# Optimization experiments

Measured on AMD Instinct MI355X. Metric: run time of the kernel, lower is better.

Reference implementation:

```python
import jax, jax.numpy as jnp
import numpy as np

NUM_HEADS = 4
D_K = 64
D_MODEL = NUM_HEADS * D_K  # 256
SEN_LEN = 8192
N_GROUPS = 4096
BASE_LEN = 64
N_EDGES = N_GROUPS * BASE_LEN  # 262144
PATH_LEN = 64


def setup_inputs() -> dict:
    rng = np.random.default_rng(0)
    key = jax.random.key(0)
    ks = jax.random.split(key, 16)

    # ragged group lengths, each >= 2, summing exactly to N_EDGES
    half = N_GROUPS // 2
    r = rng.integers(-(BASE_LEN - 2), BASE_LEN - 1, size=half)
    edge_len = np.concatenate([BASE_LEN + r, BASE_LEN - r]).astype(np.int64)
    assert edge_len.sum() == N_EDGES and edge_len.min() >= 2

    # distinct token ids; include src=0 and tar=1 so path_agg branches fire
    perm = rng.permutation(np.arange(2, SEN_LEN))[: N_GROUPS - 2]
    token_ids = np.concatenate([np.array([0, 1]), perm]).astype(np.int64)

    def w(k, shape):
        return jax.random.normal(k, shape, jnp.float32) / np.sqrt(shape[-1]).astype(np.float32)

    return {
        "path": jax.random.normal(ks[0], (PATH_LEN, D_MODEL), jnp.float32),
        "path_len": PATH_LEN,
        "q": jax.random.normal(ks[1], (SEN_LEN, D_MODEL), jnp.float32),
        "k": jax.random.normal(ks[2], (N_EDGES, D_MODEL), jnp.float32),
        "v": jax.random.normal(ks[3], (N_EDGES, D_MODEL), jnp.float32),
        "graphs": 0,
        "edge_len": jnp.asarray(edge_len),
        "token_ids": jnp.asarray(token_ids),
        "pair": jnp.array([0, 1], jnp.int32),
        "rev": 0,
        "W_qpair": w(ks[4], (D_MODEL, 2 * D_MODEL)),
        "W_pk": w(ks[5], (D_MODEL, D_MODEL)),
        "W_pv": w(ks[6], (D_MODEL, D_MODEL)),
        "W_q": w(ks[7], (D_MODEL, D_MODEL)),
        "W_k": w(ks[8], (D_MODEL, D_MODEL)),
        "W_v": w(ks[9], (D_MODEL, D_MODEL)),
        "W_out": w(ks[10], (D_MODEL, D_MODEL)),
        "b_out": jnp.zeros((D_MODEL,), jnp.float32),
        "W_agg": w(ks[11], (D_MODEL, 2 * D_MODEL)),
    }


def _forward(path, q, k, v, edge_len, token_ids, pair, rev,
             W_qpair, W_pk, W_pv, W_q, W_k, W_v, W_out, b_out, W_agg):
    H, dk = NUM_HEADS, D_K
    G = edge_len.shape[0]
    E = k.shape[0]
    scale = 1.0 / jnp.sqrt(jnp.float32(dk))

    src = pair[0] if rev == 0 else pair[1]
    tar = pair[1] if rev == 0 else pair[0]

    # pair query: cat(q[src], q[tar]) -> linear -> [H, 1, dk]
    pair_q = (jnp.concatenate([q[src], q[tar]]) @ W_qpair.T).reshape(1, H, dk).transpose(1, 0, 2)

    qh = (q @ W_q.T).reshape(-1, H, dk).transpose(1, 0, 2)      # [H, S, dk]
    pk = (path @ W_pk.T).reshape(-1, H, dk).transpose(1, 0, 2)  # [H, P, dk]
    pv = (path @ W_pv.T).reshape(-1, H, dk).transpose(1, 0, 2)  # [H, P, dk]
    kh = (k @ W_k.T).reshape(-1, H, dk).transpose(1, 0, 2)      # [H, E, dk]
    vh = (v @ W_v.T).reshape(-1, H, dk).transpose(1, 0, 2)      # [H, E, dk]

    # ---- pair/path attention ----
    att = jax.nn.softmax(jnp.einsum('hqd,hpd->hqp', pair_q, pk) * scale, axis=-1)  # [H,1,P]
    path_vals = jnp.einsum('hqp,hpd->hqd', att, pv).sum(axis=1)  # [H, dk]
    path_result = path_vals.reshape(-1) @ W_out.T + b_out        # [d_model]

    # ---- segmented per-group attention (vectorized ragged loop) ----
    seg = jnp.repeat(jnp.arange(G), edge_len, total_repeat_length=E)  # [E]
    q_sel = qh[:, token_ids, :]          # [H, G, dk] query per group
    qe = q_sel[:, seg, :]                # [H, E, dk] query per edge
    # torch.matmul(q_[H,dk], k_[H,i,dk].T) broadcasts to cross-head logits [a,b,i]
    logits = jnp.einsum('aed,bed->eab', qe, kh) * scale  # [E, H, H]
    lmax = jax.lax.stop_gradient(jax.ops.segment_max(logits, seg, num_segments=G))
    ex = jnp.exp(logits - lmax[seg])
    denom = jax.ops.segment_sum(ex, seg, num_segments=G)
    p = ex / denom[seg]                                   # segmented softmax [E, H, H]
    # sum over key-head b per edge, then segment-reduce over edges of each group
    out_e = jnp.einsum('eab,bed->ead', p, vh)             # [E, H, dk]
    hid = jax.ops.segment_sum(out_e, seg, num_segments=G) # [G, H, dk]
    new_hid = hid.reshape(G, H * dk) @ W_out.T + b_out    # [G, d_model] (dropout=identity)

    # ---- assemble output rows ----
    pr = jnp.broadcast_to(path_result, (G, D_MODEL))
    feat_path = jnp.concatenate([new_hid, pr], axis=1) @ W_agg.T  # token == src
    path_feat = jnp.concatenate([pr, new_hid], axis=1) @ W_agg.T  # token == tar
    is_src = (token_ids == src)[:, None]
    is_tar = (token_ids == tar)[:, None]
    vals = jnp.where(is_src, feat_path, jnp.where(is_tar, path_feat, new_hid))
    returned = q.at[token_ids].set(vals)
    return returned, att


def reference(path, path_len, q, k, v, graphs, edge_len, token_ids, pair, rev,
              W_qpair, W_pk, W_pv, W_q, W_k, W_v, W_out, b_out, W_agg):
    return _forward(path, q, k, v, edge_len, token_ids, pair, rev,
                    W_qpair, W_pk, W_pv, W_q, W_k, W_v, W_out, b_out, W_agg)
```

## Files before the change

### kernel.cpp

```cpp
#include <hip/hip_runtime.h>
#include <hip/hip_bf16.h>

#define H 4
#define DK 64
#define DM 256
#define SEN 8192
#define NG 4096
#define ETOT 262144
#define PLEN 64
#define MAXE 128

typedef unsigned short ushortT;
typedef __attribute__((ext_vector_type(8))) __bf16 bf16x8;
typedef __attribute__((ext_vector_type(8))) unsigned short us8;
typedef __attribute__((ext_vector_type(4))) unsigned short us4;
typedef __attribute__((ext_vector_type(4))) float f32x4;

#define TMS 264
#define KVS 260

__device__ __forceinline__ ushortT f2bf(float f) {
    unsigned u = __float_as_uint(f);
    u += 0x7FFF + ((u >> 16) & 1);
    return (ushortT)(u >> 16);
}
__device__ __forceinline__ bf16x8 ldb8(const ushortT* p) {
    us8 v = *(const us8*)p;
    return __builtin_bit_cast(bf16x8, v);
}
__device__ __forceinline__ bf16x8 pack8(const float* f) {
    us8 v;
#pragma unroll
    for (int j = 0; j < 8; j++) v[j] = f2bf(f[j]);
    return __builtin_bit_cast(bf16x8, v);
}
__device__ __forceinline__ ushortT sbf(float f) {
    return __builtin_bit_cast(ushortT, (__bf16)f);
}
__device__ __forceinline__ __bf16 u2b(ushortT u) {
    return __builtin_bit_cast(__bf16, u);
}
__device__ __forceinline__ bf16x8 pack8f(float4 a, float4 b) {
    bf16x8 r;
    r[0] = (__bf16)a.x; r[1] = (__bf16)a.y; r[2] = (__bf16)a.z; r[3] = (__bf16)a.w;
    r[4] = (__bf16)b.x; r[5] = (__bf16)b.y; r[6] = (__bf16)b.z; r[7] = (__bf16)b.w;
    return r;
}

__global__ __launch_bounds__(256) void scan_kernel(const int* __restrict__ edge_len,
                                                   int* __restrict__ starts) {
    __shared__ int part[256];
    const int tid = threadIdx.x;
    const int base = tid * 16;
    int loc[16];
    int s = 0;
#pragma unroll
    for (int i = 0; i < 16; i++) { loc[i] = s; s += edge_len[base + i]; }
    part[tid] = s;
    __syncthreads();
    if (tid == 0) {
        int acc = 0;
        for (int i = 0; i < 256; i++) { int t = part[i]; part[i] = acc; acc += t; }
    }
    __syncthreads();
    const int off = part[tid];
#pragma unroll
    for (int i = 0; i < 16; i++) starts[base + i] = off + loc[i];
}

__global__ void copy_kernel(const float* __restrict__ q, float* __restrict__ out) {
    const size_t i = (size_t)blockIdx.x * blockDim.x + threadIdx.x;
    ((float4*)out)[i] = ((const float4*)q)[i];
}

__global__ __launch_bounds__(256) void wprep_kernel(
    const float* __restrict__ W_q, const float* __restrict__ W_k,
    const float* __restrict__ W_v, const float* __restrict__ W_out,
    ushortT* __restrict__ WQb, ushortT* __restrict__ WKTb,
    ushortT* __restrict__ WVb, ushortT* __restrict__ WOb) {
    const int idx = blockIdx.x * 256 + threadIdx.x;
    const int sel = idx >> 16;
    const int i = idx & 65535;
    if (sel == 0) {
        WQb[i] = sbf(W_q[i]);
    } else if (sel == 1) {
        const int c = i >> 8, d = i & 255;
        WKTb[i] = sbf(W_k[d * DM + c]);
    } else if (sel == 2) {
        WVb[i] = sbf(W_v[i]);
    } else {
        WOb[i] = sbf(W_out[i]);
    }
}

__global__ __launch_bounds__(256) void qhtmat_kernel(
    const float* __restrict__ q, const int* __restrict__ token_ids,
    const ushortT* __restrict__ WQb, const ushortT* __restrict__ WKTb,
    ushortT* __restrict__ tmat_u) {
    __shared__ ushortT Al[16 * 264];
    __shared__ ushortT QHs[16 * 264];
    const int tid = threadIdx.x;
    const int g0 = blockIdx.x * 16;
    const int lane = tid & 63, w = tid >> 6, lq = lane & 15, lh = lane >> 4;
    {
        const int m = tid >> 4;
        const int c0 = (tid & 15) * 16;
        const int tok = token_ids[g0 + m];
        const float* qr = &q[(size_t)tok * DM + c0];
#pragma unroll
        for (int i = 0; i < 4; i++) {
            float4 v4 = *(const float4*)&qr[i * 4];
            us4 o;
            o[0] = sbf(v4.x); o[1] = sbf(v4.y); o[2] = sbf(v4.z); o[3] = sbf(v4.w);
            *(us4*)&Al[m * 264 + c0 + i * 4] = o;
        }
    }
    __syncthreads();
    {
        bf16x8 af[8];
#pragma unroll
        for (int kk = 0; kk < 8; kk++) af[kk] = ldb8(&Al[lq * 264 + kk * 32 + lh * 8]);
#pragma unroll
        for (int ntl = 0; ntl < 4; ntl++) {
            const int nt = w * 4 + ntl;
            f32x4 acc = {0.f, 0.f, 0.f, 0.f};
#pragma unroll
            for (int kk = 0; kk < 8; kk++) {
                bf16x8 bf = ldb8(&WQb[(nt * 16 + lq) * 256 + kk * 32 + lh * 8]);
                acc = __builtin_amdgcn_mfma_f32_16x16x32_bf16(af[kk], bf, acc, 0, 0, 0);
            }
#pragma unroll
            for (int r = 0; r < 4; r++)
                QHs[(lh * 4 + r) * 264 + nt * 16 + lq] = sbf(acc[r]);
        }
    }
    __syncthreads();
    for (int ab = 0; ab < 16; ab++) {
        const int a = ab >> 2, b = ab & 3;
        bf16x8 a0 = ldb8(&QHs[lq * 264 + a * 64 + lh * 8]);
        bf16x8 a1 = ldb8(&QHs[lq * 264 + a * 64 + 32 + lh * 8]);
#pragma unroll
        for (int ntl = 0; ntl < 4; ntl++) {
            const int nt = w * 4 + ntl;
            f32x4 acc = {0.f, 0.f, 0.f, 0.f};
            bf16x8 b0 = ldb8(&WKTb[(nt * 16 + lq) * 256 + b * 64 + lh * 8]);
            acc = __builtin_amdgcn_mfma_f32_16x16x32_bf16(a0, b0, acc, 0, 0, 0);
            bf16x8 b1 = ldb8(&WKTb[(nt * 16 + lq) * 256 + b * 64 + 32 + lh * 8]);
            acc = __builtin_amdgcn_mfma_f32_16x16x32_bf16(a1, b1, acc, 0, 0, 0);
#pragma unroll
            for (int r = 0; r < 4; r++)
                tmat_u[((size_t)(g0 + lh * 4 + r) * 16 + ab) * 256 + nt * 16 + lq] =
                    sbf(acc[r]);
        }
    }
}

__global__ __launch_bounds__(256, 3) void edge_kernel(
    const float* __restrict__ k, const float* __restrict__ v,
    const int* __restrict__ edge_len, const int* __restrict__ starts,
    ushortT* __restrict__ tmat_u) {
    const int g = blockIdx.x;
    const int tid = threadIdx.x;
    const float scale = 0.125f;
    __shared__ float plog[128][17];
    __shared__ ushortT pT[16 * 136];
    __shared__ float red[16][16];
    __shared__ float mx[16];
    __shared__ ushortT kvb[64 * KVS];
    const int start = starts[g];
    const int len = edge_len[g];
    const int lane = tid & 63, w = tid >> 6, lq = lane & 15, lh = lane >> 4;
    const int rg = tid >> 4, cc = tid & 15;
    const int nkc = (len + 31) >> 5;
    const int nmt = (len + 15) >> 4;
    const int col = (tid & 63) * 4;
    const int rr = tid >> 6;

    bf16x8 btm[8];
#pragma unroll
    for (int cb = 0; cb < 8; cb++)
        btm[cb] = ldb8(&tmat_u[((size_t)g * 16 + lq) * 256 + cb * 32 + lh * 8]);

    const int nch = (nmt + 3) >> 2;
    for (int c = 0; c < nch; c++) {
        const int base = c * 64;
        const int cnt = len - base;
        const int rquads = (cnt < 64 ? cnt + 3 : 67) >> 2;
#pragma unroll
        for (int i = 0; i < 16; i++) {
            if (i < rquads) {
                const int row = i * 4 + rr;
                const int gr = base + row;
                const int grc = (gr < len) ? gr : (len - 1);
                float4 v4 = *(const float4*)&k[(size_t)(start + grc) * DM + col];
                us4 o;
                o[0] = sbf(v4.x); o[1] = sbf(v4.y); o[2] = sbf(v4.z); o[3] = sbf(v4.w);
                *(us4*)&kvb[row * KVS + col] = o;
            }
        }
        __syncthreads();
        const int t = c * 4 + w;
        if (t < nmt) {
            f32x4 acc = {0.f, 0.f, 0.f, 0.f};
#pragma unroll
            for (int cb = 0; cb < 8; cb++) {
                bf16x8 ak = ldb8(&kvb[(w * 16 + lq) * KVS + cb * 32 + lh * 8]);
                acc = __builtin_amdgcn_mfma_f32_16x16x32_bf16(ak, btm[cb], acc, 0, 0, 0);
            }
#pragma unroll
            for (int r = 0; r < 4; r++) plog[t * 16 + lh * 4 + r][lq] = acc[r] * scale;
        }
        __syncthreads();
    }

    {
        float m = -3.0e38f;
        for (int e = rg; e < len; e += 16) m = fmaxf(m, plog[e][cc]);
        red[rg][cc] = m;
        __syncthreads();
        if (tid < 16) {
            float mm = red[0][tid];
            for (int i2 = 1; i2 < 16; i2++) mm = fmaxf(mm, red[i2][tid]);
            mx[tid] = mm;
        }
        __syncthreads();
        const float mm = mx[cc];
        float s = 0.f;
        for (int e = rg; e < len; e += 16) {
            float ex = __expf(plog[e][cc] - mm);
            plog[e][cc] = ex;
            s += ex;
        }
        red[rg][cc] = s;
        __syncthreads();
        if (tid < 16) {
            float ss = red[0][tid];
            for (int i2 = 1; i2 < 16; i2++) ss += red[i2][tid];
            mx[tid] = 1.0f / ss;
        }
        __syncthreads();
        const float inv = mx[cc];
        const int padlen = nkc * 32;
        for (int e = rg; e < padlen; e += 16) {
            float pv = (e < len) ? plog[e][cc] * inv : 0.f;
            pT[cc * 136 + e] = sbf(pv);
        }
    }
    __syncthreads();

    {
        f32x4 uacc[4];
#pragma unroll
        for (int nt = 0; nt < 4; nt++) uacc[nt] = {0.f, 0.f, 0.f, 0.f};
        for (int kc = 0; kc < nkc; kc++) {
            const int base = kc * 32;
#pragma unroll
            for (int i = 0; i < 8; i++) {
                const int row = i * 4 + rr;
                const int gr = base + row;
                const int grc = (gr < len) ? gr : (len - 1);
                float4 v4 = *(const float4*)&v[(size_t)(start + grc) * DM + col];
                us4 o;
                o[0] = sbf(v4.x); o[1] = sbf(v4.y); o[2] = sbf(v4.z); o[3] = sbf(v4.w);
                *(us4*)&kvb[row * KVS + col] = o;
            }
            __syncthreads();
            bf16x8 ap = ldb8(&pT[lq * 136 + kc * 32 + lh * 8]);
#pragma unroll
            for (int nt = 0; nt < 4; nt++) {
                bf16x8 bv;
#pragma unroll
                for (int j = 0; j < 8; j++)
                    bv[j] = u2b(kvb[(lh * 8 + j) * KVS + w * 64 + nt * 16 + lq]);
                uacc[nt] = __builtin_amdgcn_mfma_f32_16x16x32_bf16(ap, bv, uacc[nt], 0, 0, 0);
            }
            __syncthreads();
        }
        const int c0 = w * 64;
#pragma unroll
        for (int nt = 0; nt < 4; nt++) {
#pragma unroll
            for (int r = 0; r < 4; r++) {
                const int ab = lh * 4 + r;
                tmat_u[((size_t)g * 16 + ab) * 256 + c0 + nt * 16 + lq] = sbf(uacc[nt][r]);
            }
        }
    }
}

__global__ __launch_bounds__(256) void hidnh_kernel(
    const ushortT* __restrict__ Ub, const ushortT* __restrict__ WVb,
    const ushortT* __restrict__ WOb, const float* __restrict__ b_out,
    const int* __restrict__ token_ids, float* __restrict__ out) {
    __shared__ ushortT HIDs[16 * 264];
    const int tid = threadIdx.x;
    const int g0 = blockIdx.x * 16;
    const int lane = tid & 63, w = tid >> 6, lq = lane & 15, lh = lane >> 4;
#pragma unroll
    for (int a = 0; a < 4; a++) {
        f32x4 acc = {0.f, 0.f, 0.f, 0.f};
        for (int kk = 0; kk < 32; kk++) {
            const int kbase = kk * 32 + lh * 8;
            bf16x8 af = ldb8(&Ub[((size_t)(g0 + lq) * 16 + a * 4) * 256 + kbase]);
            bf16x8 bf = ldb8(&WVb[(size_t)((kbase >> 8) * 64 + w * 16 + lq) * 256 + (kbase & 255)]);
            acc = __builtin_amdgcn_mfma_f32_16x16x32_bf16(af, bf, acc, 0, 0, 0);
        }
#pragma unroll
        for (int r = 0; r < 4; r++)
            HIDs[(lh * 4 + r) * 264 + a * 64 + w * 16 + lq] = sbf(acc[r]);
    }
    __syncthreads();
    bf16x8 af2[8];
#pragma unroll
    for (int kk = 0; kk < 8; kk++) af2[kk] = ldb8(&HIDs[lq * 264 + kk * 32 + lh * 8]);
    int toks[4];
#pragma unroll
    for (int r = 0; r < 4; r++) toks[r] = token_ids[g0 + lh * 4 + r];
#pragma unroll
    for (int ntl = 0; ntl < 4; ntl++) {
        const int nt = w * 4 + ntl;
        f32x4 acc = {0.f, 0.f, 0.f, 0.f};
#pragma unroll
        for (int kk = 0; kk < 8; kk++) {
            bf16x8 bf = ldb8(&WOb[(nt * 16 + lq) * 256 + kk * 32 + lh * 8]);
            acc = __builtin_amdgcn_mfma_f32_16x16x32_bf16(af2[kk], bf, acc, 0, 0, 0);
        }
        const int n = nt * 16 + lq;
        const float bo = b_out[n];
#pragma unroll
        for (int r = 0; r < 4; r++)
            out[(size_t)toks[r] * DM + n] = acc[r] + bo;
    }
}

__global__ __launch_bounds__(256) void agg_kernel(
    const int* __restrict__ token_ids, const int* __restrict__ pair,
    const int* __restrict__ rev, const float* __restrict__ W_agg,
    const float* __restrict__ path_result, float* __restrict__ out) {
    __shared__ int gsrc, gtar;
    __shared__ float catS[512], catT[512];
    const int tid = threadIdx.x;
    if (tid == 0) { gsrc = -1; gtar = -1; }
    __syncthreads();
    const int rv = rev[0];
    const int src = (rv == 0) ? pair[0] : pair[1];
    const int tar = (rv == 0) ? pair[1] : pair[0];
    for (int i = tid; i < NG; i += 256) {
        const int tk = token_ids[i];
        if (tk == src) gsrc = i;
        if (tk == tar) gtar = i;
    }
    __syncthreads();
    const int gs = gsrc, gt = gtar;
    if (gs >= 0) {
        catS[tid] = out[(size_t)src * DM + tid];
        catS[256 + tid] = path_result[tid];
    }
    if (gt >= 0) {
        catT[tid] = path_result[tid];
        catT[256 + tid] = out[(size_t)tar * DM + tid];
    }
    __syncthreads();
    if (gs >= 0) {
        float acc = 0.f;
        for (int n = 0; n < 512; n += 4) {
            float4 w4 = *(const float4*)&W_agg[(size_t)tid * 512 + n];
            acc += w4.x * catS[n] + w4.y * catS[n + 1] + w4.z * catS[n + 2] + w4.w * catS[n + 3];
        }
        out[(size_t)src * DM + tid] = acc;
    }
    if (gt >= 0) {
        float acc = 0.f;
        for (int n = 0; n < 512; n += 4) {
            float4 w4 = *(const float4*)&W_agg[(size_t)tid * 512 + n];
            acc += w4.x * catT[n] + w4.y * catT[n + 1] + w4.z * catT[n + 2] + w4.w * catT[n + 3];
        }
        out[(size_t)tar * DM + tid] = acc;
    }
}

__global__ __launch_bounds__(256) void pathB_kernel(
    const float* __restrict__ path, const float* __restrict__ q,
    const int* __restrict__ pair, const int* __restrict__ rev,
    const float* __restrict__ W_qpair, const float* __restrict__ W_pk,
    const float* __restrict__ W_pv,
    float* __restrict__ pv_ws, float* __restrict__ logits_ws) {
    __shared__ float cat[512];
    __shared__ float pq[256];
    __shared__ float prow[256];
    __shared__ float lp[256];
    const int p = blockIdx.x;
    const int tid = threadIdx.x;
    const int rv = rev[0];
    const int src = (rv == 0) ? pair[0] : pair[1];
    const int tar = (rv == 0) ? pair[1] : pair[0];
    cat[tid] = q[(size_t)src * DM + tid];
    cat[256 + tid] = q[(size_t)tar * DM + tid];
    prow[tid] = path[p * DM + tid];
    __syncthreads();
    float acc = 0.f;
    for (int c = 0; c < 512; c += 4) {
        float4 w4 = *(const float4*)&W_qpair[(size_t)tid * 512 + c];
        acc += w4.x * cat[c] + w4.y * cat[c + 1] + w4.z * cat[c + 2] + w4.w * cat[c + 3];
    }
    pq[tid] = acc;
    __syncthreads();
    float pkv = 0.f, pvv = 0.f;
    for (int c = 0; c < 256; c += 4) {
        float4 a4 = *(const float4*)&W_pk[tid * DM + c];
        float4 b4 = *(const float4*)&W_pv[tid * DM + c];
        float4 x4 = *(const float4*)&prow[c];
        pkv += a4.x * x4.x + a4.y * x4.y + a4.z * x4.z + a4.w * x4.w;
        pvv += b4.x * x4.x + b4.y * x4.y + b4.z * x4.z + b4.w * x4.w;
    }
    pv_ws[p * DM + tid] = pvv;
    lp[tid] = pq[tid] * pkv;
    __syncthreads();
    if (tid < H) {
        float s = 0.f;
        for (int d = 0; d < DK; d++) s += lp[tid * DK + d];
        logits_ws[tid * PLEN + p] = s * 0.125f;
    }
}

__global__ __launch_bounds__(256) void pathC_kernel(
    const float* __restrict__ pv_ws, const float* __restrict__ logits_ws,
    const float* __restrict__ W_out, const float* __restrict__ b_out,
    float* __restrict__ att_out, float* __restrict__ path_result) {
    __shared__ float att[256];
    __shared__ float pvals[256];
    const int tid = threadIdx.x;
    att[tid] = logits_ws[tid];
    __syncthreads();
    if (tid < H) {
        float m = -3.0e38f;
        for (int p = 0; p < PLEN; p++) m = fmaxf(m, att[tid * PLEN + p]);
        float s = 0.f;
        for (int p = 0; p < PLEN; p++) {
            float e = __expf(att[tid * PLEN + p] - m);
            att[tid * PLEN + p] = e;
            s += e;
        }
        float inv = 1.f / s;
        for (int p = 0; p < PLEN; p++) att[tid * PLEN + p] *= inv;
    }
    __syncthreads();
    att_out[tid] = att[tid];
    {
        const int h = tid >> 6;
        float a = 0.f;
        for (int p = 0; p < PLEN; p++) a += att[h * PLEN + p] * pv_ws[p * DM + tid];
        pvals[tid] = a;
    }
    __syncthreads();
    {
        float a = b_out[tid];
        for (int c = 0; c < 256; c += 4) {
            float4 w4 = *(const float4*)&W_out[tid * DM + c];
            a += w4.x * pvals[c] + w4.y * pvals[c + 1] + w4.z * pvals[c + 2] + w4.w * pvals[c + 3];
        }
        path_result[tid] = a;
    }
}

__global__ __launch_bounds__(256, 4) void group_kernel(
    const float* __restrict__ q, const float* __restrict__ k, const float* __restrict__ v,
    const int* __restrict__ edge_len, const int* __restrict__ token_ids,
    const int* __restrict__ pair, const int* __restrict__ rev,
    const float* __restrict__ W_q,
    const float* __restrict__ W_k, const float* __restrict__ W_v,
    const float* __restrict__ W_out, const float* __restrict__ b_out,
    const float* __restrict__ W_agg,
    const int* __restrict__ starts, const float* __restrict__ path_result,
    float* __restrict__ out) {
    const int g = blockIdx.x;
    const int tid = threadIdx.x;
    const float scale = 0.125f;

    __shared__ float qrow[256];
    __shared__ float qh[256];
    __shared__ ushortT qh_b[4 * 72];
    __shared__ ushortT tmat_b[16 * TMS];
    __shared__ float plog[128][17];
    __shared__ ushortT pT[16 * 136];
    __shared__ ushortT u_b[4 * 1032];
    __shared__ float hid[256];
    __shared__ float nh[256];
    __shared__ float red[16][16];
    __shared__ float mx[16];

    const int tok = token_ids[g];
    const int start = starts[g];
    const int len = edge_len[g];

    const int lane = tid & 63;
    const int w = tid >> 6;
    const int lq = lane & 15;
    const int lh = lane >> 4;
    const int rg = tid >> 4;
    const int cc = tid & 15;

    qrow[tid] = q[(size_t)tok * DM + tid];
    __syncthreads();

    for (int i = 0; i < 16; i++) {
        const int r = i * 16 + rg;
        float acc = 0.f;
#pragma unroll
        for (int j4 = 0; j4 < 4; j4++) {
            const int c0 = j4 * 64 + cc * 4;
            float4 w4 = *(const float4*)&W_q[r * DM + c0];
            float4 x4 = *(const float4*)&qrow[c0];
            acc += w4.x * x4.x + w4.y * x4.y + w4.z * x4.z + w4.w * x4.w;
        }
#pragma unroll
        for (int off = 8; off; off >>= 1) acc += __shfl_down(acc, off, 16);
        if (cc == 0) qh[r] = acc;
    }
    __syncthreads();
    qh_b[(tid >> 6) * 72 + (tid & 63)] = f2bf(qh[tid]);
    __syncthreads();

    {
        const int arow = (lq < 3) ? lq : 3;
        bf16x8 aq0 = ldb8(&qh_b[arow * 72 + lh * 8]);
        bf16x8 aq1 = ldb8(&qh_b[arow * 72 + 32 + lh * 8]);
        for (int nt = 0; nt < 16; nt++) {
            const int c = nt * 16 + lq;
            f32x4 acc = {0.f, 0.f, 0.f, 0.f};
            float wf[8];
#pragma unroll
            for (int j = 0; j < 8; j++)
                wf[j] = W_k[(size_t)(w * 64 + lh * 8 + j) * DM + c];
            acc = __builtin_amdgcn_mfma_f32_16x16x32_bf16(aq0, pack8(wf), acc, 0, 0, 0);
#pragma unroll
            for (int j = 0; j < 8; j++)
                wf[j] = W_k[(size_t)(w * 64 + 32 + lh * 8 + j) * DM + c];
            acc = __builtin_amdgcn_mfma_f32_16x16x32_bf16(aq1, pack8(wf), acc, 0, 0, 0);
            if (lane < 16) {
#pragma unroll
                for (int r = 0; r < 4; r++)
                    tmat_b[(r * 4 + w) * TMS + nt * 16 + lq] = f2bf(acc[r]);
            }
        }
    }
    __syncthreads();

    {
        bf16x8 btm[8];
#pragma unroll
        for (int cb = 0; cb < 8; cb++)
            btm[cb] = ldb8(&tmat_b[lq * TMS + cb * 32 + lh * 8]);
        const int nmt = (len + 15) >> 4;
        for (int t = w; t < nmt; t += 4) {
            const int e = t * 16 + lq;
            const int ec = (e < len) ? e : (len - 1);
            const float* krow = &k[(size_t)(start + ec) * DM + lh * 8];
            f32x4 acc = {0.f, 0.f, 0.f, 0.f};
#pragma unroll
            for (int cb = 0; cb < 8; cb++) {
                float4 k0 = *(const float4*)&krow[cb * 32];
                float4 k1 = *(const float4*)&krow[cb * 32 + 4];
                float kf[8] = {k0.x, k0.y, k0.z, k0.w, k1.x, k1.y, k1.z, k1.w};
                acc = __builtin_amdgcn_mfma_f32_16x16x32_bf16(pack8(kf), btm[cb], acc, 0, 0, 0);
            }
#pragma unroll
            for (int r = 0; r < 4; r++) plog[t * 16 + lh * 4 + r][lq] = acc[r] * scale;
        }
    }
    __syncthreads();

    const int nkc = (len + 31) >> 5;
    {
        float m = -3.0e38f;
        for (int e = rg; e < len; e += 16) m = fmaxf(m, plog[e][cc]);
        red[rg][cc] = m;
        __syncthreads();
        if (tid < 16) {
            float mm = red[0][tid];
            for (int i2 = 1; i2 < 16; i2++) mm = fmaxf(mm, red[i2][tid]);
            mx[tid] = mm;
        }
        __syncthreads();
        const float mm = mx[cc];
        float s = 0.f;
        for (int e = rg; e < len; e += 16) {
            float ex = __expf(plog[e][cc] - mm);
            plog[e][cc] = ex;
            s += ex;
        }
        red[rg][cc] = s;
        __syncthreads();
        if (tid < 16) {
            float ss = red[0][tid];
            for (int i2 = 1; i2 < 16; i2++) ss += red[i2][tid];
            mx[tid] = 1.0f / ss;
        }
        __syncthreads();
        const float inv = mx[cc];
        const int padlen = nkc * 32;
        for (int e = rg; e < padlen; e += 16) {
            float pv = (e < len) ? plog[e][cc] * inv : 0.f;
            pT[cc * 136 + e] = f2bf(pv);
        }
    }
    __syncthreads();

    {
        f32x4 uacc[4];
#pragma unroll
        for (int nt = 0; nt < 4; nt++) uacc[nt] = {0.f, 0.f, 0.f, 0.f};
        const int c0 = w * 64;
#pragma unroll
        for (int kc = 0; kc < 4; kc++) {
            if (kc < nkc) {
                bf16x8 ap = ldb8(&pT[lq * 136 + kc * 32 + lh * 8]);
#pragma unroll
                for (int nt = 0; nt < 4; nt++) {
                    float bf[8];
#pragma unroll
                    for (int j = 0; j < 8; j++) {
                        int e = kc * 32 + lh * 8 + j;
                        int ecl = (e < len) ? e : (len - 1);
                        bf[j] = v[(size_t)(start + ecl) * DM + c0 + nt * 16 + lq];
                    }
                    uacc[nt] = __builtin_amdgcn_mfma_f32_16x16x32_bf16(ap, pack8(bf), uacc[nt], 0, 0, 0);
                }
            }
        }
#pragma unroll
        for (int nt = 0; nt < 4; nt++) {
#pragma unroll
            for (int r = 0; r < 4; r++) {
                const int row = lh * 4 + r;
                const int a = row >> 2, b = row & 3;
                u_b[a * 1032 + b * 256 + c0 + nt * 16 + lq] = f2bf(uacc[nt][r]);
            }
        }
    }
    __syncthreads();

    {
        const int arow = (lq < 3) ? lq : 3;
        f32x4 hacc = {0.f, 0.f, 0.f, 0.f};
        for (int kc = 0; kc < 32; kc++) {
            bf16x8 au = ldb8(&u_b[arow * 1032 + kc * 32 + lh * 8]);
            const int kk = kc * 32 + lh * 8;
            const float* wr = &W_v[(size_t)((kk >> 8) * 64 + w * 16 + lq) * DM + (kk & 255)];
            float4 w0 = *(const float4*)&wr[0];
            float4 w1 = *(const float4*)&wr[4];
            float wf[8] = {w0.x, w0.y, w0.z, w0.w, w1.x, w1.y, w1.z, w1.w};
            hacc = __builtin_amdgcn_mfma_f32_16x16x32_bf16(au, pack8(wf), hacc, 0, 0, 0);
        }
        if (lane < 16) {
#pragma unroll
            for (int r = 0; r < 4; r++) hid[r * 64 + w * 16 + lq] = hacc[r];
        }
    }
    __syncthreads();

    for (int i = 0; i < 16; i++) {
        const int m = i * 16 + rg;
        float acc = 0.f;
#pragma unroll
        for (int j4 = 0; j4 < 4; j4++) {
            const int c0 = j4 * 64 + cc * 4;
            float4 w4 = *(const float4*)&W_out[m * DM + c0];
            float4 h4 = *(const float4*)&hid[c0];
            acc += w4.x * h4.x + w4.y * h4.y + w4.z * h4.z + w4.w * h4.w;
        }
#pragma unroll
        for (int off = 8; off; off >>= 1) acc += __shfl_down(acc, off, 16);
        if (cc == 0) nh[m] = b_out[m] + acc;
    }
    __syncthreads();

    const int rv = rev[0];
    const int src = (rv == 0) ? pair[0] : pair[1];
    const int tar = (rv == 0) ? pair[1] : pair[0];
    float val;
    if (tok == src || tok == tar) {
        qrow[tid] = path_result[tid];
        __syncthreads();
        const float* x1 = (tok == src) ? nh : qrow;
        const float* x2 = (tok == src) ? qrow : nh;
        float acc = 0.f;
        for (int n = 0; n < 256; n += 4) {
            float4 w4 = *(const float4*)&W_agg[(size_t)tid * 512 + n];
            acc += w4.x * x1[n] + w4.y * x1[n + 1] + w4.z * x1[n + 2] + w4.w * x1[n + 3];
        }
        for (int n = 0; n < 256; n += 4) {
            float4 w4 = *(const float4*)&W_agg[(size_t)tid * 512 + 256 + n];
            acc += w4.x * x2[n] + w4.y * x2[n + 1] + w4.z * x2[n + 2] + w4.w * x2[n + 3];
        }
        val = acc;
    } else {
        val = nh[tid];
    }
    out[(size_t)tok * DM + tid] = val;
}

extern "C" void kernel_launch(void* const* d_in, const int* in_sizes, int n_in,
                              void* d_out, int out_size, void* d_ws, size_t ws_size,
                              hipStream_t stream) {
    const float* path    = (const float*)d_in[0];
    const float* q       = (const float*)d_in[2];
    const float* k       = (const float*)d_in[3];
    const float* v       = (const float*)d_in[4];
    const int*   edge_len  = (const int*)d_in[6];
    const int*   token_ids = (const int*)d_in[7];
    const int*   pair      = (const int*)d_in[8];
    const int*   rev       = (const int*)d_in[9];
    const float* W_qpair = (const float*)d_in[10];
    const float* W_pk    = (const float*)d_in[11];
    const float* W_pv    = (const float*)d_in[12];
    const float* W_q     = (const float*)d_in[13];
    const float* W_k     = (const float*)d_in[14];
    const float* W_v     = (const float*)d_in[15];
    const float* W_out   = (const float*)d_in[16];
    const float* b_out   = (const float*)d_in[17];
    const float* W_agg   = (const float*)d_in[18];
    float* out = (float*)d_out;

    char* base = (char*)d_ws;
    int*    starts      = (int*)(base + 0);
    float*  path_result = (float*)(base + 16384);
    float*  pv_ws       = (float*)(base + 17408);
    float*  logits_ws   = (float*)(base + 82944);
    ushortT* WQb        = (ushortT*)(base + 83968);
    ushortT* WKTb       = (ushortT*)(base + 215040);
    ushortT* WVb        = (ushortT*)(base + 346112);
    ushortT* WOb        = (ushortT*)(base + 477184);
    ushortT* tmat_u     = (ushortT*)(base + 608256);
    const size_t NEED = 608256 + 33554432;

    copy_kernel<<<dim3(2048), dim3(256), 0, stream>>>(q, out);
    scan_kernel<<<dim3(1), dim3(256), 0, stream>>>(edge_len, starts);
    pathB_kernel<<<dim3(PLEN), dim3(256), 0, stream>>>(path, q, pair, rev, W_qpair, W_pk,
                                                       W_pv, pv_ws, logits_ws);
    pathC_kernel<<<dim3(1), dim3(256), 0, stream>>>(pv_ws, logits_ws, W_out, b_out,
                                                    out + (size_t)SEN * DM, path_result);

    if (ws_size >= NEED) {
        wprep_kernel<<<dim3(1024), dim3(256), 0, stream>>>(W_q, W_k, W_v, W_out,
                                                           WQb, WKTb, WVb, WOb);
        qhtmat_kernel<<<dim3(256), dim3(256), 0, stream>>>(q, token_ids, WQb, WKTb, tmat_u);
        edge_kernel<<<dim3(NG), dim3(256), 0, stream>>>(k, v, edge_len, starts, tmat_u);
        hidnh_kernel<<<dim3(256), dim3(256), 0, stream>>>(tmat_u, WVb, WOb, b_out,
                                                          token_ids, out);
        agg_kernel<<<dim3(1), dim3(256), 0, stream>>>(token_ids, pair, rev, W_agg,
                                                      path_result, out);
    } else {
        group_kernel<<<dim3(NG), dim3(256), 0, stream>>>(q, k, v, edge_len, token_ids, pair,
                                                         rev, W_q, W_k, W_v, W_out, b_out,
                                                         W_agg, starts, path_result, out);
    }
}
```

Before: 319.7 us.

## Merge prep, path and aggregation kernels to cut launch count

The copy, weight conversion, scan and path-projection work now run as different block ranges of one prep kernel. The path softmax and output projection run as an extra block of the q/tmat kernel. The final W_agg aggregation for the src and tar rows moves into the hidden-state kernel, which keeps those rows in shared memory instead of writing them and reading them back. This goes from eight launches to four, cutting launch overhead and serial single-block tail kernels, at the cost of more divergent blocks and shared-memory use per block.

```diff
diff --git a/kernel.cpp b/kernel.cpp
--- a/kernel.cpp
+++ b/kernel.cpp
@@ -47,59 +47,139 @@
     return r;
 }
 
-__global__ __launch_bounds__(256) void scan_kernel(const int* __restrict__ edge_len,
-                                                   int* __restrict__ starts) {
-    __shared__ int part[256];
-    const int tid = threadIdx.x;
-    const int base = tid * 16;
-    int loc[16];
-    int s = 0;
-#pragma unroll
-    for (int i = 0; i < 16; i++) { loc[i] = s; s += edge_len[base + i]; }
-    part[tid] = s;
-    __syncthreads();
-    if (tid == 0) {
-        int acc = 0;
-        for (int i = 0; i < 256; i++) { int t = part[i]; part[i] = acc; acc += t; }
-    }
-    __syncthreads();
-    const int off = part[tid];
-#pragma unroll
-    for (int i = 0; i < 16; i++) starts[base + i] = off + loc[i];
-}
-
-__global__ void copy_kernel(const float* __restrict__ q, float* __restrict__ out) {
-    const size_t i = (size_t)blockIdx.x * blockDim.x + threadIdx.x;
-    ((float4*)out)[i] = ((const float4*)q)[i];
-}
-
-__global__ __launch_bounds__(256) void wprep_kernel(
+
+__global__ __launch_bounds__(256) void prep_kernel(
+    const float* __restrict__ q, float* __restrict__ out,
+    const int* __restrict__ edge_len, int* __restrict__ starts,
+    const float* __restrict__ path, const int* __restrict__ pair,
+    const int* __restrict__ rev, const float* __restrict__ W_qpair,
+    const float* __restrict__ W_pk, const float* __restrict__ W_pv,
+    float* __restrict__ pv_ws, float* __restrict__ logits_ws,
     const float* __restrict__ W_q, const float* __restrict__ W_k,
     const float* __restrict__ W_v, const float* __restrict__ W_out,
     ushortT* __restrict__ WQb, ushortT* __restrict__ WKTb,
     ushortT* __restrict__ WVb, ushortT* __restrict__ WOb) {
-    const int idx = blockIdx.x * 256 + threadIdx.x;
-    const int sel = idx >> 16;
-    const int i = idx & 65535;
-    if (sel == 0) {
-        WQb[i] = sbf(W_q[i]);
-    } else if (sel == 1) {
-        const int c = i >> 8, d = i & 255;
-        WKTb[i] = sbf(W_k[d * DM + c]);
-    } else if (sel == 2) {
-        WVb[i] = sbf(W_v[i]);
+    __shared__ int part[256];
+    __shared__ float cat[512];
+    __shared__ float pq[256];
+    __shared__ float prow[256];
+    __shared__ float lp[256];
+    const int b = blockIdx.x;
+    const int tid = threadIdx.x;
+    if (b < 2048) {
+        const size_t i = (size_t)b * 256 + tid;
+        ((float4*)out)[i] = ((const float4*)q)[i];
+    } else if (b < 3072) {
+        const int idx = (b - 2048) * 256 + tid;
+        const int sel = idx >> 16;
+        const int i = idx & 65535;
+        if (sel == 0) {
+            WQb[i] = sbf(W_q[i]);
+        } else if (sel == 1) {
+            const int c = i >> 8, d = i & 255;
+            WKTb[i] = sbf(W_k[d * DM + c]);
+        } else if (sel == 2) {
+            WVb[i] = sbf(W_v[i]);
+        } else {
+            WOb[i] = sbf(W_out[i]);
+        }
+    } else if (b == 3072) {
+        const int base = tid * 16;
+        int loc[16];
+        int s = 0;
+#pragma unroll
+        for (int i = 0; i < 16; i++) { loc[i] = s; s += edge_len[base + i]; }
+        part[tid] = s;
+        __syncthreads();
+        if (tid == 0) {
+            int acc = 0;
+            for (int i = 0; i < 256; i++) { int t = part[i]; part[i] = acc; acc += t; }
+        }
+        __syncthreads();
+        const int off = part[tid];
+#pragma unroll
+        for (int i = 0; i < 16; i++) starts[base + i] = off + loc[i];
     } else {
-        WOb[i] = sbf(W_out[i]);
-    }
-}
-
-__global__ __launch_bounds__(256) void qhtmat_kernel(
+        const int p = b - 3073;
+        const int rv = rev[0];
+        const int src = (rv == 0) ? pair[0] : pair[1];
+        const int tar = (rv == 0) ? pair[1] : pair[0];
+        cat[tid] = q[(size_t)src * DM + tid];
+        cat[256 + tid] = q[(size_t)tar * DM + tid];
+        prow[tid] = path[p * DM + tid];
+        __syncthreads();
+        float acc = 0.f;
+        for (int c = 0; c < 512; c += 4) {
+            float4 w4 = *(const float4*)&W_qpair[(size_t)tid * 512 + c];
+            acc += w4.x * cat[c] + w4.y * cat[c + 1] + w4.z * cat[c + 2] + w4.w * cat[c + 3];
+        }
+        pq[tid] = acc;
+        __syncthreads();
+        float pkv = 0.f, pvv = 0.f;
+        for (int c = 0; c < 256; c += 4) {
+            float4 a4 = *(const float4*)&W_pk[tid * DM + c];
+            float4 b4 = *(const float4*)&W_pv[tid * DM + c];
+            float4 x4 = *(const float4*)&prow[c];
+            pkv += a4.x * x4.x + a4.y * x4.y + a4.z * x4.z + a4.w * x4.w;
+            pvv += b4.x * x4.x + b4.y * x4.y + b4.z * x4.z + b4.w * x4.w;
+        }
+        pv_ws[p * DM + tid] = pvv;
+        lp[tid] = pq[tid] * pkv;
+        __syncthreads();
+        if (tid < H) {
+            float s = 0.f;
+            for (int d = 0; d < DK; d++) s += lp[tid * DK + d];
+            logits_ws[tid * PLEN + p] = s * 0.125f;
+        }
+    }
+}
+
+__global__ __launch_bounds__(256) void qhtmatC_kernel(
     const float* __restrict__ q, const int* __restrict__ token_ids,
     const ushortT* __restrict__ WQb, const ushortT* __restrict__ WKTb,
-    ushortT* __restrict__ tmat_u) {
+    ushortT* __restrict__ tmat_u,
+    const float* __restrict__ pv_ws, const float* __restrict__ logits_ws,
+    const float* __restrict__ W_out, const float* __restrict__ b_out,
+    float* __restrict__ att_out, float* __restrict__ path_result) {
     __shared__ ushortT Al[16 * 264];
     __shared__ ushortT QHs[16 * 264];
+    __shared__ float att[256];
+    __shared__ float pvals[256];
     const int tid = threadIdx.x;
+    if (blockIdx.x == 256) {
+        att[tid] = logits_ws[tid];
+        __syncthreads();
+        if (tid < H) {
+            float m = -3.0e38f;
+            for (int p = 0; p < PLEN; p++) m = fmaxf(m, att[tid * PLEN + p]);
+            float s = 0.f;
+            for (int p = 0; p < PLEN; p++) {
+                float e = __expf(att[tid * PLEN + p] - m);
+                att[tid * PLEN + p] = e;
+                s += e;
+            }
+            float inv = 1.f / s;
+            for (int p = 0; p < PLEN; p++) att[tid * PLEN + p] *= inv;
+        }
+        __syncthreads();
+        att_out[tid] = att[tid];
+        {
+            const int h = tid >> 6;
+            float a = 0.f;
+            for (int p = 0; p < PLEN; p++) a += att[h * PLEN + p] * pv_ws[p * DM + tid];
+            pvals[tid] = a;
+        }
+        __syncthreads();
+        {
+            float a = b_out[tid];
+            for (int c = 0; c < 256; c += 4) {
+                float4 w4 = *(const float4*)&W_out[tid * DM + c];
+                a += w4.x * pvals[c] + w4.y * pvals[c + 1] + w4.z * pvals[c + 2] + w4.w * pvals[c + 3];
+            }
+            path_result[tid] = a;
+        }
+        return;
+    }
     const int g0 = blockIdx.x * 16;
     const int lane = tid & 63, w = tid >> 6, lq = lane & 15, lh = lane >> 4;
     {
@@ -136,16 +216,16 @@
     }
     __syncthreads();
     for (int ab = 0; ab < 16; ab++) {
-        const int a = ab >> 2, b = ab & 3;
+        const int a = ab >> 2, bb = ab & 3;
         bf16x8 a0 = ldb8(&QHs[lq * 264 + a * 64 + lh * 8]);
         bf16x8 a1 = ldb8(&QHs[lq * 264 + a * 64 + 32 + lh * 8]);
 #pragma unroll
         for (int ntl = 0; ntl < 4; ntl++) {
             const int nt = w * 4 + ntl;
             f32x4 acc = {0.f, 0.f, 0.f, 0.f};
-            bf16x8 b0 = ldb8(&WKTb[(nt * 16 + lq) * 256 + b * 64 + lh * 8]);
+            bf16x8 b0 = ldb8(&WKTb[(nt * 16 + lq) * 256 + bb * 64 + lh * 8]);
             acc = __builtin_amdgcn_mfma_f32_16x16x32_bf16(a0, b0, acc, 0, 0, 0);
-            bf16x8 b1 = ldb8(&WKTb[(nt * 16 + lq) * 256 + b * 64 + 32 + lh * 8]);
+            bf16x8 b1 = ldb8(&WKTb[(nt * 16 + lq) * 256 + bb * 64 + 32 + lh * 8]);
             acc = __builtin_amdgcn_mfma_f32_16x16x32_bf16(a1, b1, acc, 0, 0, 0);
 #pragma unroll
             for (int r = 0; r < 4; r++)
@@ -288,14 +368,21 @@
     }
 }
 
-__global__ __launch_bounds__(256) void hidnh_kernel(
+__global__ __launch_bounds__(256) void hidnhagg_kernel(
     const ushortT* __restrict__ Ub, const ushortT* __restrict__ WVb,
     const ushortT* __restrict__ WOb, const float* __restrict__ b_out,
-    const int* __restrict__ token_ids, float* __restrict__ out) {
+    const int* __restrict__ token_ids, const int* __restrict__ pair,
+    const int* __restrict__ rev, const float* __restrict__ W_agg,
+    const float* __restrict__ path_result, float* __restrict__ out) {
     __shared__ ushortT HIDs[16 * 264];
+    __shared__ float nhs[2][260];
+    __shared__ float prb[256];
+    __shared__ int flagrow[2];
     const int tid = threadIdx.x;
     const int g0 = blockIdx.x * 16;
     const int lane = tid & 63, w = tid >> 6, lq = lane & 15, lh = lane >> 4;
+    if (tid < 2) flagrow[tid] = -1;
+    prb[tid] = path_result[tid];
 #pragma unroll
     for (int a = 0; a < 4; a++) {
         f32x4 acc = {0.f, 0.f, 0.f, 0.f};
@@ -313,9 +400,16 @@
     bf16x8 af2[8];
 #pragma unroll
     for (int kk = 0; kk < 8; kk++) af2[kk] = ldb8(&HIDs[lq * 264 + kk * 32 + lh * 8]);
+    const int rv = rev[0];
+    const int src = (rv == 0) ? pair[0] : pair[1];
+    const int tar = (rv == 0) ? pair[1] : pair[0];
     int toks[4];
 #pragma unroll
-    for (int r = 0; r < 4; r++) toks[r] = token_ids[g0 + lh * 4 + r];
+    for (int r = 0; r < 4; r++) {
+        toks[r] = token_ids[g0 + lh * 4 + r];
+        if (toks[r] == src) flagrow[0] = lh * 4 + r;
+        else if (toks[r] == tar) flagrow[1] = lh * 4 + r;
+    }
 #pragma unroll
     for (int ntl = 0; ntl < 4; ntl++) {
         const int nt = w * 4 + ntl;
@@ -328,55 +422,58 @@
         const int n = nt * 16 + lq;
         const float bo = b_out[n];
 #pragma unroll
-        for (int r = 0; r < 4; r++)
-            out[(size_t)toks[r] * DM + n] = acc[r] + bo;
-    }
-}
-
-__global__ __launch_bounds__(256) void agg_kernel(
-    const int* __restrict__ token_ids, const int* __restrict__ pair,
-    const int* __restrict__ rev, const float* __restrict__ W_agg,
-    const float* __restrict__ path_result, float* __restrict__ out) {
-    __shared__ int gsrc, gtar;
-    __shared__ float catS[512], catT[512];
+        for (int r = 0; r < 4; r++) {
+            const float val = acc[r] + bo;
+            if (toks[r] == src) nhs[0][n] = val;
+            else if (toks[r] == tar) nhs[1][n] = val;
+            else out[(size_t)toks[r] * DM + n] = val;
+        }
+    }
+    __syncthreads();
+#pragma unroll
+    for (int s = 0; s < 2; s++) {
+        if (flagrow[s] >= 0) {
+            const float* x1 = (s == 0) ? nhs[0] : prb;
+            const float* x2 = (s == 0) ? prb : nhs[1];
+            float acc = 0.f;
+            for (int n = 0; n < 256; n += 4) {
+                float4 w4 = *(const float4*)&W_agg[(size_t)tid * 512 + n];
+                acc += w4.x * x1[n] + w4.y * x1[n + 1] + w4.z * x1[n + 2] + w4.w * x1[n + 3];
+            }
+            for (int n = 0; n < 256; n += 4) {
+                float4 w4 = *(const float4*)&W_agg[(size_t)tid * 512 + 256 + n];
+                acc += w4.x * x2[n] + w4.y * x2[n + 1] + w4.z * x2[n + 2] + w4.w * x2[n + 3];
+            }
+            out[(size_t)((s == 0) ? src : tar) * DM + tid] = acc;
+        }
+    }
+}
+
+
+__global__ __launch_bounds__(256) void scan_kernel(const int* __restrict__ edge_len,
+                                                   int* __restrict__ starts) {
+    __shared__ int part[256];
     const int tid = threadIdx.x;
-    if (tid == 0) { gsrc = -1; gtar = -1; }
-    __syncthreads();
-    const int rv = rev[0];
-    const int src = (rv == 0) ? pair[0] : pair[1];
-    const int tar = (rv == 0) ? pair[1] : pair[0];
-    for (int i = tid; i < NG; i += 256) {
-        const int tk = token_ids[i];
-        if (tk == src) gsrc = i;
-        if (tk == tar) gtar = i;
-    }
-    __syncthreads();
-    const int gs = gsrc, gt = gtar;
-    if (gs >= 0) {
-        catS[tid] = out[(size_t)src * DM + tid];
-        catS[256 + tid] = path_result[tid];
-    }
-    if (gt >= 0) {
-        catT[tid] = path_result[tid];
-        catT[256 + tid] = out[(size_t)tar * DM + tid];
-    }
-    __syncthreads();
-    if (gs >= 0) {
-        float acc = 0.f;
-        for (int n = 0; n < 512; n += 4) {
-            float4 w4 = *(const float4*)&W_agg[(size_t)tid * 512 + n];
-            acc += w4.x * catS[n] + w4.y * catS[n + 1] + w4.z * catS[n + 2] + w4.w * catS[n + 3];
-        }
-        out[(size_t)src * DM + tid] = acc;
-    }
-    if (gt >= 0) {
-        float acc = 0.f;
-        for (int n = 0; n < 512; n += 4) {
-            float4 w4 = *(const float4*)&W_agg[(size_t)tid * 512 + n];
-            acc += w4.x * catT[n] + w4.y * catT[n + 1] + w4.z * catT[n + 2] + w4.w * catT[n + 3];
-        }
-        out[(size_t)tar * DM + tid] = acc;
-    }
+    const int base = tid * 16;
+    int loc[16];
+    int s = 0;
+#pragma unroll
+    for (int i = 0; i < 16; i++) { loc[i] = s; s += edge_len[base + i]; }
+    part[tid] = s;
+    __syncthreads();
+    if (tid == 0) {
+        int acc = 0;
+        for (int i = 0; i < 256; i++) { int t = part[i]; part[i] = acc; acc += t; }
+    }
+    __syncthreads();
+    const int off = part[tid];
+#pragma unroll
+    for (int i = 0; i < 16; i++) starts[base + i] = off + loc[i];
+}
+
+__global__ void copy_kernel(const float* __restrict__ q, float* __restrict__ out) {
+    const size_t i = (size_t)blockIdx.x * blockDim.x + threadIdx.x;
+    ((float4*)out)[i] = ((const float4*)q)[i];
 }
 
 __global__ __launch_bounds__(256) void pathB_kernel(
@@ -734,23 +831,23 @@
     ushortT* tmat_u     = (ushortT*)(base + 608256);
     const size_t NEED = 608256 + 33554432;
 
-    copy_kernel<<<dim3(2048), dim3(256), 0, stream>>>(q, out);
-    scan_kernel<<<dim3(1), dim3(256), 0, stream>>>(edge_len, starts);
-    pathB_kernel<<<dim3(PLEN), dim3(256), 0, stream>>>(path, q, pair, rev, W_qpair, W_pk,
-                                                       W_pv, pv_ws, logits_ws);
-    pathC_kernel<<<dim3(1), dim3(256), 0, stream>>>(pv_ws, logits_ws, W_out, b_out,
-                                                    out + (size_t)SEN * DM, path_result);
-
     if (ws_size >= NEED) {
-        wprep_kernel<<<dim3(1024), dim3(256), 0, stream>>>(W_q, W_k, W_v, W_out,
-                                                           WQb, WKTb, WVb, WOb);
-        qhtmat_kernel<<<dim3(256), dim3(256), 0, stream>>>(q, token_ids, WQb, WKTb, tmat_u);
+        prep_kernel<<<dim3(3137), dim3(256), 0, stream>>>(
+            q, out, edge_len, starts, path, pair, rev, W_qpair, W_pk, W_pv,
+            pv_ws, logits_ws, W_q, W_k, W_v, W_out, WQb, WKTb, WVb, WOb);
+        qhtmatC_kernel<<<dim3(257), dim3(256), 0, stream>>>(
+            q, token_ids, WQb, WKTb, tmat_u, pv_ws, logits_ws, W_out, b_out,
+            out + (size_t)SEN * DM, path_result);
         edge_kernel<<<dim3(NG), dim3(256), 0, stream>>>(k, v, edge_len, starts, tmat_u);
-        hidnh_kernel<<<dim3(256), dim3(256), 0, stream>>>(tmat_u, WVb, WOb, b_out,
-                                                          token_ids, out);
-        agg_kernel<<<dim3(1), dim3(256), 0, stream>>>(token_ids, pair, rev, W_agg,
-                                                      path_result, out);
+        hidnhagg_kernel<<<dim3(256), dim3(256), 0, stream>>>(
+            tmat_u, WVb, WOb, b_out, token_ids, pair, rev, W_agg, path_result, out);
     } else {
+        copy_kernel<<<dim3(2048), dim3(256), 0, stream>>>(q, out);
+        scan_kernel<<<dim3(1), dim3(256), 0, stream>>>(edge_len, starts);
+        pathB_kernel<<<dim3(PLEN), dim3(256), 0, stream>>>(path, q, pair, rev, W_qpair,
+                                                           W_pk, W_pv, pv_ws, logits_ws);
+        pathC_kernel<<<dim3(1), dim3(256), 0, stream>>>(pv_ws, logits_ws, W_out, b_out,
+                                                        out + (size_t)SEN * DM, path_result);
         group_kernel<<<dim3(NG), dim3(256), 0, stream>>>(q, k, v, edge_len, token_ids, pair,
                                                          rev, W_q, W_k, W_v, W_out, b_out,
                                                          W_agg, starts, path_result, out);
```

New measurement: 301.4 us. -5.7%, faster.
